# Performance work log

Hardware: AMD Instinct MI355X
Metric: run time of the kernel (lower is better)

The kernel has to match this reference:

```python
import jax, jax.numpy as jnp
import numpy as np

B, N, C = 4, 2048, 512
H = 8  # num_heads
HD = C // H  # head_dim = 64


def setup_inputs() -> dict:
    key = jax.random.key(0)
    k_x, k_qkv, k_w, k_b = jax.random.split(key, 4)
    x = jax.random.normal(k_x, (B, N, C), dtype=jnp.float32)
    # torch nn.Linear weights are stored as (out_features, in_features)
    w_qkv = jax.random.normal(k_qkv, (3 * C, C), dtype=jnp.float32) * 0.02  # bias=False
    w_proj = jax.random.normal(k_w, (C, C), dtype=jnp.float32) * 0.02
    b_proj = jax.random.normal(k_b, (C,), dtype=jnp.float32) * 0.02
    return {"x": x, "w_qkv": w_qkv, "w_proj": w_proj, "b_proj": b_proj}


def reference(x, w_qkv, w_proj, b_proj):
    b, n, c = x.shape
    scale = HD ** -0.5
    # QKV projection (no bias): (B,N,C) @ (C,3C) -> (B,N,3C)
    qkv = jnp.einsum('bnc,dc->bnd', x, w_qkv)
    qkv = qkv.reshape(b, n, 3, H, HD).transpose(2, 0, 3, 1, 4)  # (3,B,H,N,HD)
    q, k, v = qkv[0], qkv[1], qkv[2]
    # scaled dot-product attention, full N x N scores
    attn = jnp.einsum('bhqd,bhkd->bhqk', q, k) * scale
    attn = jax.nn.softmax(attn, axis=-1)
    out = jnp.einsum('bhqk,bhkd->bhqd', attn, v)  # (B,H,N,HD)
    out = out.transpose(0, 2, 1, 3).reshape(b, n, c)  # (B,N,C)
    # output projection with bias
    return jnp.einsum('bnc,dc->bnd', out, w_proj) + b_proj
```

## Files before the change

kernel.cpp:

```cpp
#include <hip/hip_runtime.h>

typedef _Float16 f16;
typedef _Float16 f16x4 __attribute__((ext_vector_type(4)));
typedef _Float16 f16x8 __attribute__((ext_vector_type(8)));
typedef __fp16 fp16x2 __attribute__((ext_vector_type(2)));
typedef float f32x4 __attribute__((ext_vector_type(4)));

static __device__ __forceinline__ f32x4 mfma_k32(f16x8 a, f16x8 b, f32x4 c) {
  return __builtin_amdgcn_mfma_f32_16x16x32_f16(a, b, c, 0, 0, 0);
}
static __device__ __forceinline__ f32x4 mfma_k16(f16x4 a, f16x4 b, f32x4 c) {
  return __builtin_amdgcn_mfma_f32_16x16x16f16(a, b, c, 0, 0, 0);
}
static __device__ __forceinline__ void gll16(const f16* g, f16* l) {
  __builtin_amdgcn_global_load_lds(
      (const __attribute__((address_space(1))) void*)g,
      (__attribute__((address_space(3))) void*)l, 16, 0, 0);
}

#define BN 2048
#define CC 512
#define NHD 64
#define MROWS 8192
#define SLAB ((size_t)32 * BN * NHD)
#define CH 64
#define QSCALE 0.1803368801111204f

__global__ __launch_bounds__(256)
void cvt_f16(const float* __restrict__ X, const float* __restrict__ Wq,
             const float* __restrict__ Wp, f16* __restrict__ x16,
             f16* __restrict__ wq16, f16* __restrict__ wp16) {
  const int idx = blockIdx.x * 256 + threadIdx.x;
  const int stride = gridDim.x * 256;
  for (int i = idx; i < (MROWS * CC) / 4; i += stride) {
    float4 v = ((const float4*)X)[i];
    f16x4 h = {(f16)v.x, (f16)v.y, (f16)v.z, (f16)v.w};
    ((f16x4*)x16)[i] = h;
  }
  for (int i = idx; i < (3 * CC * CC) / 4; i += stride) {
    float4 v = ((const float4*)Wq)[i];
    f16x4 h = {(f16)v.x, (f16)v.y, (f16)v.z, (f16)v.w};
    ((f16x4*)wq16)[i] = h;
  }
  for (int i = idx; i < (CC * CC) / 4; i += stride) {
    float4 v = ((const float4*)Wp)[i];
    f16x4 h = {(f16)v.x, (f16)v.y, (f16)v.z, (f16)v.w};
    ((f16x4*)wp16)[i] = h;
  }
}

__global__ __launch_bounds__(256)
void qkv_gemm(const f16* __restrict__ X, const f16* __restrict__ W,
              f16* __restrict__ qkv) {
  __shared__ __align__(16) f16 As[128 * 32];
  __shared__ __align__(16) f16 Bs[128 * 32];
  const int t = threadIdx.x;
  const int lane = t & 63, wave = t >> 6;
  const int wr = wave >> 1, wc = wave & 1;
  const int mt = blockIdx.x / 12, nt = blockIdx.x % 12;
  const int m0 = mt * 128, n0 = nt * 128;
  const int grp = lane >> 4, lid = lane & 15;

  const int srow = 32 * wave + (lane >> 2);
  const int gslot = (lane & 3) ^ ((lane >> 2) & 3);
  const int ga0 = (m0 + srow) * CC + gslot * 8;
  const int gb0 = (n0 + srow) * CC + gslot * 8;
  f16* const ldsA = As + wave * 1024;
  f16* const ldsB = Bs + wave * 1024;

  const int abase = wr * 2048 + lid * 32 + (grp ^ (lid & 3)) * 8;
  const int bbase = wc * 2048 + lid * 32 + (grp ^ (lid & 3)) * 8;

  const f32x4 zf = {0.f, 0.f, 0.f, 0.f};
  f32x4 acc[4][4];
#pragma unroll
  for (int i = 0; i < 4; i++)
#pragma unroll
    for (int j = 0; j < 4; j++) acc[i][j] = zf;

  for (int k0 = 0; k0 < CC; k0 += 32) {
    gll16(X + ga0 + k0, ldsA);
    gll16(X + ga0 + 16 * CC + k0, ldsA + 512);
    gll16(W + gb0 + k0, ldsB);
    gll16(W + gb0 + 16 * CC + k0, ldsB + 512);
    __syncthreads();
    f16x8 af[4], bf[4];
#pragma unroll
    for (int mi = 0; mi < 4; mi++)
      af[mi] = *(const f16x8*)&As[abase + mi * 512];
#pragma unroll
    for (int ni = 0; ni < 4; ni++)
      bf[ni] = *(const f16x8*)&Bs[bbase + ni * 512];
#pragma unroll
    for (int mi = 0; mi < 4; mi++)
#pragma unroll
      for (int ni = 0; ni < 4; ni++)
        acc[mi][ni] = mfma_k32(af[mi], bf[ni], acc[mi][ni]);
    __syncthreads();
  }
#pragma unroll
  for (int ni = 0; ni < 4; ni++) {
    int d = n0 + wc * 64 + ni * 16 + lid;
    int s = d >> 9;
    int h = (d & 511) >> 6;
    int hd = d & 63;
    if (s == 2) {
#pragma unroll
      for (int mi = 0; mi < 4; mi++) {
        int row0 = m0 + wr * 64 + mi * 16 + grp * 4;
        int b = row0 >> 11, n = row0 & 2047;
        f16x4 pk = {(f16)acc[mi][ni][0], (f16)acc[mi][ni][1],
                    (f16)acc[mi][ni][2], (f16)acc[mi][ni][3]};
        *(f16x4*)&qkv[2 * SLAB + ((size_t)((b * 8 + h) * 64 + hd)) * BN + n] = pk;
      }
    } else {
      float scale = (s == 0) ? QSCALE : 1.0f;
#pragma unroll
      for (int mi = 0; mi < 4; mi++) {
#pragma unroll
        for (int i = 0; i < 4; i++) {
          int row = m0 + wr * 64 + mi * 16 + grp * 4 + i;
          int b = row >> 11, n = row & 2047;
          qkv[(size_t)s * SLAB + (((size_t)(b * 8 + h) * BN + n)) * NHD + hd] =
              (f16)(acc[mi][ni][i] * scale);
        }
      }
    }
  }
}

__global__ __launch_bounds__(256)
void attn(const f16* __restrict__ qkv, f16* __restrict__ O) {
  __shared__ __align__(16) char smem[32768];

  const int bh = blockIdx.x & 31;
  const int qb = blockIdx.x >> 5;
  const f16* Q = qkv + (size_t)bh * BN * NHD;
  const f16* K = qkv + SLAB + (size_t)bh * BN * NHD;
  const f16* VT = qkv + 2 * SLAB + (size_t)bh * (size_t)NHD * BN;
  const int t = threadIdx.x, lane = t & 63, wave = t >> 6;
  const int grp = lane >> 4, qv = lane & 15;
  const int qrow = qb * 64 + wave * 16 + qv;
  const int xr = (qv & 7) << 4;

  char* const kaddr0 = smem + qv * 128 + ((grp * 16) ^ xr);
  char* const kaddr1 = smem + qv * 128 + ((grp * 16 + 64) ^ xr);
  char* const va0 = smem + qv * 128 + ((0 * 32 + grp * 8) ^ xr);
  char* const va1 = smem + qv * 128 + ((1 * 32 + grp * 8) ^ xr);
  char* const va2 = smem + qv * 128 + ((2 * 32 + grp * 8) ^ xr);
  char* const va3 = smem + qv * 128 + ((3 * 32 + grp * 8) ^ xr);

  const int srow = wave * 16 + (lane >> 3);
  const int scol = (lane & 7) ^ (lane >> 3);
  const int lo_k0 = srow * NHD + scol * 8;
  const int lo_k1 = (srow + 8) * NHD + scol * 8;
  const int lo_v0 = srow * BN + scol * 8;
  const int lo_v1 = (srow + 8) * BN + scol * 8;
  f16* const dK = (f16*)(smem + wave * 2048);
  f16* const dV = (f16*)(smem + 16384 + wave * 2048);

  f16x8 qf0 = *(const f16x8*)(Q + (size_t)qrow * NHD + grp * 8);
  f16x8 qf1 = *(const f16x8*)(Q + (size_t)qrow * NHD + 32 + grp * 8);

  const f32x4 zf = {0.f, 0.f, 0.f, 0.f};
  const f16x4 ones = {(f16)1.f, (f16)1.f, (f16)1.f, (f16)1.f};
  f32x4 acc[4];
#pragma unroll
  for (int i = 0; i < 4; i++) acc[i] = zf;
  f32x4 lacc = zf;

  int koff = 0, voff = 0;
  gll16(K + lo_k0, dK);
  gll16(K + lo_k1, dK + 512);
  gll16(VT + lo_v0, dV);
  gll16(VT + lo_v1, dV + 512);
  koff = CH * NHD; voff = CH;
  __syncthreads();

#define ATTN_BODY(BUF, PF)                                                    \
  {                                                                           \
    if (PF) {                                                                 \
      gll16(K + koff + lo_k0, dK + (BUF ^ 1) * 4096);                         \
      gll16(K + koff + lo_k1, dK + (BUF ^ 1) * 4096 + 512);                   \
      gll16(VT + voff + lo_v0, dV + (BUF ^ 1) * 4096);                        \
      gll16(VT + voff + lo_v1, dV + (BUF ^ 1) * 4096 + 512);                  \
      koff += CH * NHD; voff += CH;                                           \
    }                                                                         \
    __builtin_amdgcn_s_setprio(1);                                            \
    _Pragma("unroll")                                                         \
    for (int kt = 0; kt < 4; kt++) {                                          \
      f16x8 k0v = *(const f16x8*)(kaddr0 + BUF * 8192 + kt * 2048);           \
      f16x8 k1v = *(const f16x8*)(kaddr1 + BUF * 8192 + kt * 2048);           \
      f32x4 st = mfma_k32(k1v, qf1, mfma_k32(k0v, qf0, zf));                  \
      union { f16x4 v; fp16x2 h[2]; } u;                                      \
      u.h[0] = __builtin_amdgcn_cvt_pkrtz(exp2f(st[0]), exp2f(st[1]));        \
      u.h[1] = __builtin_amdgcn_cvt_pkrtz(exp2f(st[2]), exp2f(st[3]));        \
      f16x4 pb = u.v;                                                         \
      lacc = mfma_k16(ones, pb, lacc);                                        \
      const char* vak = (kt == 0) ? va0 : (kt == 1) ? va1 : (kt == 2) ? va2 : va3; \
      _Pragma("unroll")                                                       \
      for (int dt = 0; dt < 4; dt++) {                                        \
        f16x4 vf = *(const f16x4*)(vak + 16384 + BUF * 8192 + dt * 2048);     \
        acc[dt] = mfma_k16(vf, pb, acc[dt]);                                  \
      }                                                                       \
    }                                                                         \
    __builtin_amdgcn_s_setprio(0);                                            \
    __syncthreads();                                                          \
  }

  for (int p = 0; p < 15; ++p) {
    ATTN_BODY(0, 1)
    ATTN_BODY(1, 1)
  }
  ATTN_BODY(0, 1)
  ATTN_BODY(1, 0)
#undef ATTN_BODY

  const int b = bh >> 3, h = bh & 7;
  float inv = 1.0f / lacc[0];
#pragma unroll
  for (int dt = 0; dt < 4; dt++) {
    f16x4 o = {(f16)(acc[dt][0] * inv), (f16)(acc[dt][1] * inv),
               (f16)(acc[dt][2] * inv), (f16)(acc[dt][3] * inv)};
    *(f16x4*)&O[((size_t)(b * BN + qrow)) * CC + h * NHD + dt * 16 + grp * 4] = o;
  }
}

__global__ __launch_bounds__(256)
void proj_gemm(const f16* __restrict__ A, const f16* __restrict__ W,
               const float* __restrict__ bias, float* __restrict__ out) {
  __shared__ __align__(16) f16 As[128 * 32];
  __shared__ __align__(16) f16 Bs[128 * 32];
  const int t = threadIdx.x;
  const int lane = t & 63, wave = t >> 6;
  const int wr = wave >> 1, wc = wave & 1;
  const int mt = blockIdx.x >> 2, nt = blockIdx.x & 3;
  const int m0 = mt * 128, n0 = nt * 128;
  const int grp = lane >> 4, lid = lane & 15;

  const int srow = 32 * wave + (lane >> 2);
  const int gslot = (lane & 3) ^ ((lane >> 2) & 3);
  const int ga0 = (m0 + srow) * CC + gslot * 8;
  const int gb0 = (n0 + srow) * CC + gslot * 8;
  f16* const ldsA = As + wave * 1024;
  f16* const ldsB = Bs + wave * 1024;
  const int abase = wr * 2048 + lid * 32 + (grp ^ (lid & 3)) * 8;
  const int bbase = wc * 2048 + lid * 32 + (grp ^ (lid & 3)) * 8;

  const f32x4 zf = {0.f, 0.f, 0.f, 0.f};
  f32x4 acc[4][4];
#pragma unroll
  for (int i = 0; i < 4; i++)
#pragma unroll
    for (int j = 0; j < 4; j++) acc[i][j] = zf;

  for (int k0 = 0; k0 < CC; k0 += 32) {
    gll16(A + ga0 + k0, ldsA);
    gll16(A + ga0 + 16 * CC + k0, ldsA + 512);
    gll16(W + gb0 + k0, ldsB);
    gll16(W + gb0 + 16 * CC + k0, ldsB + 512);
    __syncthreads();
    f16x8 af[4], bf[4];
#pragma unroll
    for (int mi = 0; mi < 4; mi++)
      af[mi] = *(const f16x8*)&As[abase + mi * 512];
#pragma unroll
    for (int ni = 0; ni < 4; ni++)
      bf[ni] = *(const f16x8*)&Bs[bbase + ni * 512];
#pragma unroll
    for (int mi = 0; mi < 4; mi++)
#pragma unroll
      for (int ni = 0; ni < 4; ni++)
        acc[mi][ni] = mfma_k32(af[mi], bf[ni], acc[mi][ni]);
    __syncthreads();
  }
#pragma unroll
  for (int mi = 0; mi < 4; mi++) {
#pragma unroll
    for (int ni = 0; ni < 4; ni++) {
      int d = n0 + wc * 64 + ni * 16 + lid;
      float bv = bias[d];
#pragma unroll
      for (int i = 0; i < 4; i++) {
        int row = m0 + wr * 64 + mi * 16 + grp * 4 + i;
        out[(size_t)row * CC + d] = acc[mi][ni][i] + bv;
      }
    }
  }
}

extern "C" void kernel_launch(void* const* d_in, const int* in_sizes, int n_in,
                              void* d_out, int out_size, void* d_ws, size_t ws_size,
                              hipStream_t stream) {
  const float* x = (const float*)d_in[0];
  const float* w_qkv = (const float*)d_in[1];
  const float* w_proj = (const float*)d_in[2];
  const float* b_proj = (const float*)d_in[3];
  float* out = (float*)d_out;

  f16* qkv = (f16*)d_ws;
  f16* Obuf = qkv + 3 * SLAB;
  f16* x16 = Obuf;
  f16* wq16 = Obuf + (size_t)MROWS * CC;
  f16* wp16 = wq16 + (size_t)3 * CC * CC;

  cvt_f16<<<dim3(1024), dim3(256), 0, stream>>>(x, w_qkv, w_proj, x16, wq16, wp16);
  qkv_gemm<<<dim3(64 * 12), dim3(256), 0, stream>>>(x16, wq16, qkv);
  attn<<<dim3(32 * 32), dim3(256), 0, stream>>>(qkv, Obuf);
  proj_gemm<<<dim3(64 * 4), dim3(256), 0, stream>>>(Obuf, wp16, b_proj, out);
}
```

Baseline: 113.6 us.

## Permute V^T layout for 16-byte LDS reads and stage Q/K epilogue through LDS

```diff
diff --git a/kernel.cpp b/kernel.cpp
--- a/kernel.cpp
+++ b/kernel.cpp
@@ -54,6 +54,7 @@
               f16* __restrict__ qkv) {
   __shared__ __align__(16) f16 As[128 * 32];
   __shared__ __align__(16) f16 Bs[128 * 32];
+  __shared__ __align__(16) f16 ep[64 * 130];
   const int t = threadIdx.x;
   const int lane = t & 63, wave = t >> 6;
   const int wr = wave >> 1, wc = wave & 1;
@@ -98,33 +99,51 @@
         acc[mi][ni] = mfma_k32(af[mi], bf[ni], acc[mi][ni]);
     __syncthreads();
   }
-#pragma unroll
-  for (int ni = 0; ni < 4; ni++) {
-    int d = n0 + wc * 64 + ni * 16 + lid;
-    int s = d >> 9;
-    int h = (d & 511) >> 6;
-    int hd = d & 63;
-    if (s == 2) {
+
+  const int s = n0 >> 9;
+  if (s == 2) {
+#pragma unroll
+    for (int ni = 0; ni < 4; ni++) {
+      int d = n0 + wc * 64 + ni * 16 + lid;
+      int h = (d & 511) >> 6;
+      int hd = d & 63;
 #pragma unroll
       for (int mi = 0; mi < 4; mi++) {
         int row0 = m0 + wr * 64 + mi * 16 + grp * 4;
-        int b = row0 >> 11, n = row0 & 2047;
+        int b = row0 >> 11, nA = row0 & 2047;
+        int posA = (nA & ~31) | (((nA >> 2) & 3) << 3) | (((nA >> 4) & 1) << 2);
         f16x4 pk = {(f16)acc[mi][ni][0], (f16)acc[mi][ni][1],
                     (f16)acc[mi][ni][2], (f16)acc[mi][ni][3]};
-        *(f16x4*)&qkv[2 * SLAB + ((size_t)((b * 8 + h) * 64 + hd)) * BN + n] = pk;
+        *(f16x4*)&qkv[2 * SLAB + ((size_t)((b * 8 + h) * 64 + hd)) * BN + posA] = pk;
       }
-    } else {
-      float scale = (s == 0) ? QSCALE : 1.0f;
-#pragma unroll
-      for (int mi = 0; mi < 4; mi++) {
-#pragma unroll
-        for (int i = 0; i < 4; i++) {
-          int row = m0 + wr * 64 + mi * 16 + grp * 4 + i;
-          int b = row >> 11, n = row & 2047;
-          qkv[(size_t)s * SLAB + (((size_t)(b * 8 + h) * BN + n)) * NHD + hd] =
-              (f16)(acc[mi][ni][i] * scale);
-        }
+    }
+  } else {
+    const float scale = (s == 0) ? QSCALE : 1.0f;
+#pragma unroll
+    for (int ph = 0; ph < 2; ++ph) {
+      if (wr == ph) {
+#pragma unroll
+        for (int mi = 0; mi < 4; mi++)
+#pragma unroll
+          for (int ni = 0; ni < 4; ni++)
+#pragma unroll
+            for (int i = 0; i < 4; i++)
+              ep[(mi * 16 + grp * 4 + i) * 130 + wc * 64 + ni * 16 + lid] =
+                  (f16)(acc[mi][ni][i] * scale);
       }
+      __syncthreads();
+#pragma unroll
+      for (int u = 0; u < 4; ++u) {
+        int unit = t + u * 256;
+        int row = unit >> 4, seg = unit & 15;
+        int row_g = m0 + ph * 64 + row;
+        int b = row_g >> 11, n = row_g & 2047;
+        int d_g = n0 + seg * 8;
+        int h = (d_g & 511) >> 6, hd = d_g & 63;
+        f16x8 v = *(const f16x8*)&ep[row * 130 + seg * 8];
+        *(f16x8*)&qkv[(size_t)s * SLAB + ((size_t)((b * 8 + h) * BN + n)) * 64 + hd] = v;
+      }
+      __syncthreads();
     }
   }
 }
@@ -145,10 +164,6 @@
 
   char* const kaddr0 = smem + qv * 128 + ((grp * 16) ^ xr);
   char* const kaddr1 = smem + qv * 128 + ((grp * 16 + 64) ^ xr);
-  char* const va0 = smem + qv * 128 + ((0 * 32 + grp * 8) ^ xr);
-  char* const va1 = smem + qv * 128 + ((1 * 32 + grp * 8) ^ xr);
-  char* const va2 = smem + qv * 128 + ((2 * 32 + grp * 8) ^ xr);
-  char* const va3 = smem + qv * 128 + ((3 * 32 + grp * 8) ^ xr);
 
   const int srow = wave * 16 + (lane >> 3);
   const int scol = (lane & 7) ^ (lane >> 3);
@@ -188,20 +203,28 @@
     }                                                                         \
     __builtin_amdgcn_s_setprio(1);                                            \
     _Pragma("unroll")                                                         \
-    for (int kt = 0; kt < 4; kt++) {                                          \
-      f16x8 k0v = *(const f16x8*)(kaddr0 + BUF * 8192 + kt * 2048);           \
-      f16x8 k1v = *(const f16x8*)(kaddr1 + BUF * 8192 + kt * 2048);           \
-      f32x4 st = mfma_k32(k1v, qf1, mfma_k32(k0v, qf0, zf));                  \
-      union { f16x4 v; fp16x2 h[2]; } u;                                      \
-      u.h[0] = __builtin_amdgcn_cvt_pkrtz(exp2f(st[0]), exp2f(st[1]));        \
-      u.h[1] = __builtin_amdgcn_cvt_pkrtz(exp2f(st[2]), exp2f(st[3]));        \
-      f16x4 pb = u.v;                                                         \
-      lacc = mfma_k16(ones, pb, lacc);                                        \
-      const char* vak = (kt == 0) ? va0 : (kt == 1) ? va1 : (kt == 2) ? va2 : va3; \
+    for (int kt2 = 0; kt2 < 2; kt2++) {                                       \
+      char* const ka = kt2 ? kaddr1 : kaddr0;                                 \
+      f16x8 k0a = *(const f16x8*)(kaddr0 + BUF * 8192 + kt2 * 4096);          \
+      f16x8 k1a = *(const f16x8*)(kaddr1 + BUF * 8192 + kt2 * 4096);          \
+      f32x4 st0 = mfma_k32(k1a, qf1, mfma_k32(k0a, qf0, zf));                 \
+      f16x8 k0b = *(const f16x8*)(kaddr0 + BUF * 8192 + kt2 * 4096 + 2048);   \
+      f16x8 k1b = *(const f16x8*)(kaddr1 + BUF * 8192 + kt2 * 4096 + 2048);   \
+      f32x4 st1 = mfma_k32(k1b, qf1, mfma_k32(k0b, qf0, zf));                 \
+      union { f16x4 v; fp16x2 h[2]; } u0, u1;                                 \
+      u0.h[0] = __builtin_amdgcn_cvt_pkrtz(exp2f(st0[0]), exp2f(st0[1]));     \
+      u0.h[1] = __builtin_amdgcn_cvt_pkrtz(exp2f(st0[2]), exp2f(st0[3]));     \
+      u1.h[0] = __builtin_amdgcn_cvt_pkrtz(exp2f(st1[0]), exp2f(st1[1]));     \
+      u1.h[1] = __builtin_amdgcn_cvt_pkrtz(exp2f(st1[2]), exp2f(st1[3]));     \
+      f16x4 pb0 = u0.v, pb1 = u1.v;                                           \
+      lacc = mfma_k16(ones, pb0, lacc);                                       \
+      lacc = mfma_k16(ones, pb1, lacc);                                       \
       _Pragma("unroll")                                                       \
       for (int dt = 0; dt < 4; dt++) {                                        \
-        f16x4 vf = *(const f16x4*)(vak + 16384 + BUF * 8192 + dt * 2048);     \
-        acc[dt] = mfma_k16(vf, pb, acc[dt]);                                  \
+        union { f16x8 w; f16x4 h4[2]; } uv;                                   \
+        uv.w = *(const f16x8*)(ka + 16384 + BUF * 8192 + dt * 2048);          \
+        acc[dt] = mfma_k16(uv.h4[0], pb0, acc[dt]);                           \
+        acc[dt] = mfma_k16(uv.h4[1], pb1, acc[dt]);                           \
       }                                                                       \
     }                                                                         \
     __builtin_amdgcn_s_setprio(0);                                            \
```

Result: faster. 110.8 us (-2.4%).
